# Performance work log

Hardware: AMD Instinct MI355X
Metric: run time of the kernel (lower is better)

Reference implementation:

```python
import jax, jax.numpy as jnp
import numpy as np

B, N, C, D, K, H, A = 4, 2048, 128, 128, 16, 64, 512


def _rn(k, shape, s):
    return (jax.random.normal(k, shape) * s).astype(jnp.float32)


def setup_inputs():
    ks = jax.random.split(jax.random.key(0), 40)
    w = lambda i, o, c: _rn(ks[i], (o, c), 0.02)
    b = lambda i, o: _rn(ks[i + 20], (o,), 0.02)
    p = {}
    p["xyz"] = _rn(ks[0], (B, 3, N), 1.0)
    p["pos"] = _rn(ks[1], (B, 2, N), 1.0)
    p["key"] = _rn(ks[2], (B, C, N), 1.0)
    p["query"] = _rn(ks[3], (B, C, N), 1.0)
    p["mv_w1"] = w(4, C, 2 * C); p["mv_b1"] = b(4, C)
    p["mv_w2"] = w(5, C, C);     p["mv_b2"] = b(5, C)
    p["mv_ws"] = w(6, C, 2 * C); p["mv_bs"] = b(6, C)
    p["wk"] = w(7, D, C); p["bk"] = b(7, D)
    p["wq"] = w(8, D, C); p["bq"] = b(8, D)
    p["wv"] = w(9, D, C); p["bv"] = b(9, D)
    p["xyz_w1"] = w(10, H, 3); p["xyz_b1"] = b(10, H)
    p["xyz_w2"] = w(11, D, H); p["xyz_b2"] = b(11, D)
    p["pos_w1"] = w(12, H, 2); p["pos_b1"] = b(12, H)
    p["pos_w2"] = w(13, D, H); p["pos_b2"] = b(13, D)
    p["xat_w1"] = w(14, A, D); p["xat_b1"] = b(14, A)
    p["xat_w2"] = w(15, D, A); p["xat_b2"] = b(15, D)
    p["at_w1"] = w(16, A, D); p["at_b1"] = b(16, A)
    p["at_w2"] = w(17, D, A); p["at_b2"] = b(17, D)
    p["wkq"] = w(18, C, D); p["bkq"] = b(18, C)
    p["wend"] = w(19, C, D); p["bend"] = b(19, C)
    return p


def c1(w, b, x):  # 1x1 Conv1d: (O,C) on (B,C,N)
    return jnp.einsum('oc,bcn->bon', w, x) + b[None, :, None]


def c2(w, b, x):  # 1x1 Conv2d: (O,C) on (B,C,N,K)
    return jnp.einsum('oc,bcnk->bonk', w, x) + b[None, :, None, None]


def mlp2(w1, b1, w2, b2, x):
    return c2(w2, b2, jax.nn.relu(c2(w1, b1, x)))


def softmax_one(x):  # exp(x-m) / (1 + sum exp(x-m)) over last axis
    m = jnp.max(x, axis=-1, keepdims=True)
    e = jnp.exp(x - m)
    return e / (1.0 + jnp.sum(e, axis=-1, keepdims=True))


def knn_idx(pts, k):  # pts: (B, N, d) -> (B, N, k) indices, include_self=True
    sq = jnp.sum(pts * pts, axis=-1)
    d2 = sq[:, :, None] + sq[:, None, :] - 2.0 * jnp.einsum('bnd,bmd->bnm', pts, pts)
    return jnp.argsort(d2, axis=-1)[:, :, :k]


def group(f, idx):  # f: (B,C,N), idx: (B,N,K) -> (B,C,N,K)
    return jax.vmap(lambda a, i: a[:, i])(f, idx)


def reference(xyz, pos, key, query, mv_w1, mv_b1, mv_w2, mv_b2, mv_ws, mv_bs,
              wk, bk, wq, bq, wv, bv, xyz_w1, xyz_b1, xyz_w2, xyz_b2,
              pos_w1, pos_b1, pos_w2, pos_b2, xat_w1, xat_b1, xat_w2, xat_b2,
              at_w1, at_b1, at_w2, at_b2, wkq, bkq, wend, bend):
    cat = jnp.concatenate([key, query], axis=1)  # (B, 2C, N)
    # MLP_Res
    value = c1(mv_w2, mv_b2, jax.nn.relu(c1(mv_w1, mv_b1, cat))) + c1(mv_ws, mv_bs, cat)
    identity = value
    k = c1(wk, bk, key)
    q = c1(wq, bq, query)
    v = c1(wv, bv, value)
    # ---- block 1: xyz-space kNN attention ----
    idx1 = knn_idx(jnp.swapaxes(xyz, 1, 2), K)           # (B,N,K)
    kq_rel = k[..., None] - group(q, idx1)               # (B,D,N,K)
    xyz_rel = xyz[..., None] - group(xyz, idx1)          # (B,3,N,K)
    xyz_emb = mlp2(xyz_w1, xyz_b1, xyz_w2, xyz_b2, xyz_rel)
    xa = softmax_one(mlp2(xat_w1, xat_b1, xat_w2, xat_b2, kq_rel + xyz_emb))
    agg = jnp.sum(xa * (v[..., None] + xyz_emb), axis=-1)  # (B,D,N)
    value = c1(wkq, bkq, agg) + identity
    value = c1(wv, bv, value)
    # ---- block 2: pos-space kNN attention ----
    idx2 = knn_idx(jnp.swapaxes(pos, 1, 2), K)
    qk_rel = q[..., None] - group(k, idx2)
    pos_rel = pos[..., None] - group(pos, idx2)
    pos_emb = mlp2(pos_w1, pos_b1, pos_w2, pos_b2, pos_rel)
    at = softmax_one(mlp2(at_w1, at_b1, at_w2, at_b2, qk_rel + pos_emb))
    agg = jnp.sum(at * (value[..., None] + pos_emb), axis=-1)
    y = c1(wend, bend, agg)
    return y + identity
```

## Files before the change

### kernel.cpp

```cpp
#include <hip/hip_runtime.h>
#include <hip/hip_bf16.h>

typedef __hip_bfloat16 bf16;
typedef unsigned long long ull;

#define BB 4
#define NN 2048
#define CCH 128
#define DDM 128
#define KNB 16
#define HHD 64
#define AAD 512
#define PP (BB*NN)

typedef __attribute__((ext_vector_type(8))) short short8;
typedef __attribute__((ext_vector_type(16))) float f32x16;

__device__ __forceinline__ float b2f(bf16 x) { return __bfloat162float(x); }
__device__ __forceinline__ bf16 f2b(float x) { return __float2bfloat16(x); }

__device__ __forceinline__ float ldany(const void* p, size_t i, int f32) {
  return f32 ? ((const float*)p)[i] : __bfloat162float(((const bf16*)p)[i]);
}

__device__ __forceinline__ long pack4(float a, float b, float c, float d) {
  union { bf16 h[4]; long l; } u;
  u.h[0] = f2b(a); u.h[1] = f2b(b); u.h[2] = f2b(c); u.h[3] = f2b(d);
  return u.l;
}
__device__ __forceinline__ void unpack4(long l, float* o) {
  union { bf16 h[4]; long l; } u; u.l = l;
  o[0] = b2f(u.h[0]); o[1] = b2f(u.h[1]); o[2] = b2f(u.h[2]); o[3] = b2f(u.h[3]);
}

__device__ __forceinline__ short8 ldfrag(const bf16* base, int row, int stride, int k0, int hl) {
  const bf16* p = base + (size_t)row * stride + k0 + (hl << 3);
  union { short8 v; long l[2]; } u;
  u.l[0] = *(const long*)p;
  u.l[1] = *(const long*)(p + 4);
  return u.v;
}

__device__ __forceinline__ f32x16 MFMA(short8 a, short8 b, f32x16 c) {
  return __builtin_amdgcn_mfma_f32_32x32x16_bf16(a, b, c, 0, 0, 0);
}

struct PtrArr { const void* p[36]; int n[36]; };
struct CvtTab { int src[16]; int off[16]; int n[16]; int isb[16]; };
struct G4 { const bf16* X[4]; int K[4]; int woff[4]; int boff[4]; bf16* out[4]; int relu[4]; };

__global__ __launch_bounds__(256) void sniff_kern(PtrArr pa, int* __restrict__ flags) {
  int t = blockIdx.x;
  const bf16* x = (const bf16*)pa.p[t];
  int n = pa.n[t]; if (n > 4096) n = 4096;
  __shared__ int cnt;
  if (threadIdx.x == 0) cnt = 0;
  __syncthreads();
  int c = 0;
  for (int i = threadIdx.x; i < n; i += 256) {
    float v = fabsf(__bfloat162float(x[i]));
    if (v == 0.f || (v >= 1e-6f && v <= 1024.f)) c++;
  }
  atomicAdd(&cnt, c);
  __syncthreads();
  if (threadIdx.x == 0) flags[t] = (cnt >= (n * 7) / 8) ? 0 : 1;
}

__global__ __launch_bounds__(256) void cvtprep_kern(PtrArr pa, CvtTab tab,
                                                    const int* __restrict__ flags,
                                                    bf16* __restrict__ warena, float* __restrict__ barena,
                                                    bf16* __restrict__ w1img0, bf16* __restrict__ w2img0,
                                                    bf16* __restrict__ cw2img0, float* __restrict__ fb0,
                                                    bf16* __restrict__ w1img1, bf16* __restrict__ w2img1,
                                                    bf16* __restrict__ cw2img1, float* __restrict__ fb1) {
  int y = blockIdx.y;
  if (y >= 2) {
    int e = y - 2;
    int i = blockIdx.x * 256 + threadIdx.x;
    if (i >= tab.n[e]) return;
    float v = ldany(pa.p[tab.src[e]], i, flags[tab.src[e]]);
    if (tab.isb[e]) barena[tab.off[e] + i] = v;
    else warena[tab.off[e] + i] = f2b(v);
    return;
  }
  int set = y;
  int cIdx = set ? 20 : 16, aIdx = set ? 28 : 24, dd = set ? 2 : 3;
  bf16* w1img = set ? w1img1 : w1img0;
  bf16* w2img = set ? w2img1 : w2img0;
  bf16* cw2img = set ? cw2img1 : cw2img0;
  float* fb = set ? fb1 : fb0;
  const void* cw1 = pa.p[cIdx];     const void* cb1 = pa.p[cIdx + 1];
  const void* cw2 = pa.p[cIdx + 2]; const void* cb2 = pa.p[cIdx + 3];
  const void* aw1 = pa.p[aIdx];     const void* ab1 = pa.p[aIdx + 1];
  const void* aw2 = pa.p[aIdx + 2]; const void* ab2 = pa.p[aIdx + 3];
  int i = blockIdx.x * 256 + threadIdx.x;
  const int fcw1 = flags[cIdx], fcb1 = flags[cIdx + 1];
  const int fcw2 = flags[cIdx + 2], fcb2 = flags[cIdx + 3];
  const int faw1 = flags[aIdx], fab1 = flags[aIdx + 1];
  const int faw2 = flags[aIdx + 2], fab2 = flags[aIdx + 3];
  float* ab1f = fb;
  float* ab2f = fb + 512;
  float* cb1f = fb + 640;
  float* cb2f = fb + 704;
  float* cw1f = fb + 832;
  if (i < 65536) {
    int hg = i >> 7, c = i & 127;
    w1img[(size_t)hg * 132 + c] = f2b(ldany(aw1, i, faw1));
  } else if (i < 131072) {
    int j = i - 65536;
    int o = j >> 9, hh = j & 511;
    int ac = hh >> 7, hloc = hh & 127;
    w2img[(size_t)(ac * 128 + o) * 132 + hloc] = f2b(ldany(aw2, j, faw2));
  } else if (i < 139264) {
    int j = i - 131072;
    int o = j >> 6, h = j & 63;
    cw2img[o * 68 + h] = f2b(ldany(cw2, j, fcw2));
  } else if (i < 139776) {
    int j = i - 139264; ab1f[j] = ldany(ab1, j, fab1);
  } else if (i < 139904) {
    int j = i - 139776; ab2f[j] = ldany(ab2, j, fab2);
  } else if (i < 139968) {
    int j = i - 139904; cb1f[j] = ldany(cb1, j, fcb1);
  } else if (i < 140096) {
    int j = i - 139968; cb2f[j] = ldany(cb2, j, fcb2);
  } else if (i < 140288) {
    int j = i - 140096;
    int h = j / 3, c = j % 3;
    cw1f[j] = (c < dd) ? ldany(cw1, h * dd + c, fcw1) : 0.f;
  }
}

__global__ __launch_bounds__(256) void trall_kern(const void* __restrict__ keyp,
                                                  const void* __restrict__ qryp,
                                                  const void* __restrict__ xyzp,
                                                  const void* __restrict__ posp,
                                                  const int* __restrict__ flags,
                                                  bf16* __restrict__ catT,
                                                  float* __restrict__ xyzT,
                                                  float* __restrict__ posT) {
  int bx = blockIdx.x;
  if (bx < 512) {
    __shared__ float tile[64][65];
    int xx = bx & 31, yy = (bx >> 5) & 1, zz = bx >> 6;
    int b = zz & 3, half = zz >> 2;
    const void* src = half ? qryp : keyp;
    const int f32 = flags[2 + half];
    int n0 = xx * 64, c0 = yy * 64;
    int tx = threadIdx.x & 63, ty = threadIdx.x >> 6;
    for (int r = ty; r < 64; r += 4)
      tile[r][tx] = ldany(src, (size_t)(b * 128 + c0 + r) * NN + n0 + tx, f32);
    __syncthreads();
    for (int r = ty; r < 64; r += 4)
      catT[(size_t)(b * NN + n0 + r) * 256 + half * 128 + c0 + tx] = __float2bfloat16(tile[tx][r]);
    return;
  }
  int cb = bx - 512;
  int which = cb >> 7;
  const void* src = which ? posp : xyzp;
  float* dst = which ? posT : xyzT;
  int dd = which ? 2 : 3;
  const int f32 = flags[which];
  int i = (cb & 127) * 256 * 2 + threadIdx.x;
  for (int rep = 0; rep < 2; ++rep, i += 256) {
    if (i < PP * 4) {
      int p = i >> 2, j = i & 3;
      int b = p >> 11, n = p & (NN - 1);
      dst[i] = (j < dd) ? ldany(src, (size_t)(b * dd + j) * NN + n, f32) : 0.f;
    }
  }
}

__global__ __launch_bounds__(256) void gemm4_kern(G4 g, const bf16* __restrict__ warena,
                                                  const float* __restrict__ barena) {
  __shared__ __attribute__((aligned(16))) bf16 XT[64 * 260];
  int op = blockIdx.y;
  const bf16* X = g.X[op];
  int K = g.K[op];
  const bf16* Wb = warena + g.woff[op];
  const float* bias = barena + g.boff[op];
  bf16* out = g.out[op];
  int relu = g.relu[op];
  int tid = threadIdx.x, lane = tid & 63, wv = tid >> 6;
  int hl = lane >> 5, cA = lane & 31;
  int p0 = blockIdx.x * 64;
  int SK = K + 4;
  int kc = K >> 3;
  for (int c = tid; c < 64 * kc; c += 256) {
    int r = c / kc, col = (c % kc) << 3;
    *(float4*)&XT[r * SK + col] = *(const float4*)&X[(size_t)(p0 + r) * 256 + col];
  }
  __syncthreads();
  int o0 = wv * 32;
  f32x16 acc[2];
#pragma unroll
  for (int r = 0; r < 16; ++r) {
    int o = o0 + (r & 3) + 8 * (r >> 2) + 4 * hl;
    float bv = bias[o];
    acc[0][r] = bv; acc[1][r] = bv;
  }
  for (int ks = 0; ks < (K >> 4); ++ks) {
    short8 af = ldfrag(Wb, o0 + cA, K, ks * 16, hl);
    short8 b0 = ldfrag(XT, cA, SK, ks * 16, hl);
    short8 b1 = ldfrag(XT, 32 + cA, SK, ks * 16, hl);
    acc[0] = MFMA(af, b0, acc[0]);
    acc[1] = MFMA(af, b1, acc[1]);
  }
#pragma unroll
  for (int t = 0; t < 2; ++t) {
    int m = p0 + t * 32 + cA;
#pragma unroll
    for (int q = 0; q < 4; ++q) {
      int ob = o0 + 8 * q + 4 * hl;
      float v[4] = {acc[t][4*q+0], acc[t][4*q+1], acc[t][4*q+2], acc[t][4*q+3]};
      if (relu) {
        v[0] = fmaxf(v[0], 0.f); v[1] = fmaxf(v[1], 0.f);
        v[2] = fmaxf(v[2], 0.f); v[3] = fmaxf(v[3], 0.f);
      }
      *(long*)(out + (size_t)m * 128 + ob) = pack4(v[0], v[1], v[2], v[3]);
    }
  }
}

__global__ __launch_bounds__(256) void gemm32_kern(
    const bf16* __restrict__ X,
    const bf16* __restrict__ Wb, const float* __restrict__ bias,
    const bf16* __restrict__ add, bf16* __restrict__ out, int relu,
    void* __restrict__ outT, const int* __restrict__ flags) {
  __shared__ __attribute__((aligned(16))) bf16 XT[32 * 132];
  int tid = threadIdx.x, lane = tid & 63, wv = tid >> 6;
  int hl = lane >> 5, cA = lane & 31;
  int p0 = blockIdx.x * 32;
  for (int c = tid; c < 32 * 16; c += 256) {
    int r = c >> 4, col = (c & 15) << 3;
    *(float4*)&XT[r * 132 + col] = *(const float4*)&X[(size_t)(p0 + r) * 128 + col];
  }
  __syncthreads();
  int o0 = wv * 32;
  f32x16 acc;
#pragma unroll
  for (int r = 0; r < 16; ++r) {
    int o = o0 + (r & 3) + 8 * (r >> 2) + 4 * hl;
    acc[r] = bias[o];
  }
#pragma unroll
  for (int ks = 0; ks < 8; ++ks) {
    short8 af = ldfrag(Wb, o0 + cA, 128, ks * 16, hl);
    short8 b0 = ldfrag(XT, cA, 132, ks * 16, hl);
    acc = MFMA(af, b0, acc);
  }
  int m = p0 + cA;
  int f32o = outT ? flags[2] : 0;
  int b = m >> 11, n = m & (NN - 1);
#pragma unroll
  for (int q = 0; q < 4; ++q) {
    int ob = o0 + 8 * q + 4 * hl;
    float v[4] = {acc[4*q+0], acc[4*q+1], acc[4*q+2], acc[4*q+3]};
    if (add) {
      float av[4];
      unpack4(*(const long*)(add + (size_t)m * 128 + ob), av);
      v[0] += av[0]; v[1] += av[1]; v[2] += av[2]; v[3] += av[3];
    }
    if (relu) {
      v[0] = fmaxf(v[0], 0.f); v[1] = fmaxf(v[1], 0.f);
      v[2] = fmaxf(v[2], 0.f); v[3] = fmaxf(v[3], 0.f);
    }
    if (outT) {
#pragma unroll
      for (int i = 0; i < 4; ++i) {
        size_t oi = (size_t)(b * 128 + ob + i) * NN + n;
        if (f32o) ((float*)outT)[oi] = v[i];
        else ((bf16*)outT)[oi] = f2b(v[i]);
      }
    } else {
      *(long*)(out + (size_t)m * 128 + ob) = pack4(v[0], v[1], v[2], v[3]);
    }
  }
}

__global__ __launch_bounds__(512) void knn_kern(const float* __restrict__ xyzT,
                                                const float* __restrict__ posT,
                                                int* __restrict__ idx1,
                                                int* __restrict__ idx2) {
  __shared__ __attribute__((aligned(16))) float4 cds[NN];
  const float* coordsT = blockIdx.y ? posT : xyzT;
  int* idxout = blockIdx.y ? idx2 : idx1;
  int tid = threadIdx.x, lane = tid & 63, wv = tid >> 6;
  int p0 = blockIdx.x * 8, b = p0 >> 11;
  for (int j = tid; j < NN; j += 512)
    cds[j] = *(const float4*)&coordsT[((size_t)(b << 11) + j) * 4];
  __syncthreads();
  int p = p0 + wv, n = p & (NN - 1);
  float4 cc = cds[n];
  float sqi = __fadd_rn(__fadd_rn(__fmul_rn(cc.x, cc.x), __fmul_rn(cc.y, cc.y)),
                        __fmul_rn(cc.z, cc.z));
  ull t[32];
#pragma unroll
  for (int s = 0; s < 32; ++s) {
    int j = (s << 6) | lane;
    float4 q = cds[j];
    float sqj = __fadd_rn(__fadd_rn(__fmul_rn(q.x, q.x), __fmul_rn(q.y, q.y)),
                          __fmul_rn(q.z, q.z));
    float dt  = __fadd_rn(__fadd_rn(__fmul_rn(cc.x, q.x), __fmul_rn(cc.y, q.y)),
                          __fmul_rn(cc.z, q.z));
    float d2 = __fsub_rn(__fadd_rn(sqi, sqj), __fmul_rn(2.f, dt));
    unsigned u = __float_as_uint(d2);
    u = (u & 0x80000000u) ? ~u : (u | 0x80000000u);
    t[s] = ((ull)u << 32) | (unsigned)j;
  }
#pragma unroll
  for (int k = 2; k <= 32; k <<= 1) {
#pragma unroll
    for (int j = k >> 1; j > 0; j >>= 1) {
#pragma unroll
      for (int i = 0; i < 32; ++i) {
        int l = i ^ j;
        if (l > i) {
          bool up = ((i & k) == 0);
          ull a = t[i], c = t[l];
          ull lo = a < c ? a : c;
          ull hi = a < c ? c : a;
          t[i] = up ? lo : hi;
          t[l] = up ? hi : lo;
        }
      }
    }
  }
  for (int r = 0; r < KNB; ++r) {
    ull h = t[0];
    ull m = h;
#pragma unroll
    for (int off = 1; off < 64; off <<= 1) {
      ull o = __shfl_xor(m, off);
      m = o < m ? o : m;
    }
    if (lane == 0) idxout[(size_t)p * KNB + r] = (int)(m & 0xffffffffu);
    if (h == m) {
#pragma unroll
      for (int i = 0; i < 15; ++i) t[i] = t[i + 1];
      t[15] = ~0ull;
    }
  }
}

#define SMEM_BYTES 72192
__global__ __launch_bounds__(512, 4) void attn_mfma(
    const bf16* __restrict__ centerT, const bf16* __restrict__ gatherT,
    const float* __restrict__ coordsT, const bf16* __restrict__ vfeatT,
    const int* __restrict__ idx,
    const bf16* __restrict__ w1img, const bf16* __restrict__ w2img,
    const bf16* __restrict__ cw2img, const float* __restrict__ fb,
    bf16* __restrict__ aggT) {
  extern __shared__ char smem[];
  bf16* XS  = (bf16*)(smem);
  bf16* HT  = (bf16*)(smem + 33792);
  bf16* HC  = HT;
  bf16* CFE = (bf16*)(smem + 67584);
  bf16* VF  = (bf16*)(smem + 69632);
  int*  NID = (int*)(smem + 71680);
  const float* ab1f = fb;
  const float* ab2f = fb + 512;
  const float* cb1f = fb + 640;
  const float* cb2f = fb + 704;
  const float* cw1f = fb + 832;

  int tid = threadIdx.x, lane = tid & 63, wv = tid >> 6;
  int hl = lane >> 5, cA = lane & 31;
  int P0 = blockIdx.x * 8, b = P0 >> 11;

  if (tid < 128) NID[tid] = (b << 11) + idx[(size_t)(P0 + (tid >> 4)) * KNB + (tid & 15)];
  for (int i = tid; i < 1024; i += 512) {
    int g = i >> 7, d = i & 127;
    CFE[i] = centerT[(size_t)(P0 + g) * 128 + d];
    VF[i]  = vfeatT[(size_t)(P0 + g) * 128 + d];
  }
  __syncthreads();

  {
    int m = tid >> 2, sub = tid & 3;
    float4 ccd = *(const float4*)&coordsT[(size_t)(P0 + (m >> 4)) * 4];
    float4 nbd = *(const float4*)&coordsT[(size_t)NID[m] * 4];
    float r0 = ccd.x - nbd.x, r1 = ccd.y - nbd.y, r2 = ccd.z - nbd.z;
    int h0 = sub * 16;
    for (int hh = h0; hh < h0 + 16; hh += 4) {
      float a0 = fmaxf(cb1f[hh+0] + cw1f[(hh+0)*3]*r0 + cw1f[(hh+0)*3+1]*r1 + cw1f[(hh+0)*3+2]*r2, 0.f);
      float a1 = fmaxf(cb1f[hh+1] + cw1f[(hh+1)*3]*r0 + cw1f[(hh+1)*3+1]*r1 + cw1f[(hh+1)*3+2]*r2, 0.f);
      float a2 = fmaxf(cb1f[hh+2] + cw1f[(hh+2)*3]*r0 + cw1f[(hh+2)*3+1]*r1 + cw1f[(hh+2)*3+2]*r2, 0.f);
      float a3 = fmaxf(cb1f[hh+3] + cw1f[(hh+3)*3]*r0 + cw1f[(hh+3)*3+1]*r1 + cw1f[(hh+3)*3+2]*r2, 0.f);
      *(long*)&HC[m * 68 + hh] = pack4(a0, a1, a2, a3);
    }
    const bf16* grow = gatherT + (size_t)NID[m] * 128 + sub * 32;
    const bf16* crow = CFE + ((m >> 4) << 7) + sub * 32;
    for (int j = 0; j < 32; j += 4) {
      float gv[4], cv[4];
      unpack4(*(const long*)(grow + j), gv);
      unpack4(*(const long*)(crow + j), cv);
      *(long*)&XS[m * 132 + sub * 32 + j] =
          pack4(cv[0] - gv[0], cv[1] - gv[1], cv[2] - gv[2], cv[3] - gv[3]);
    }
  }
  __syncthreads();

  int r0s = (wv & 3) * 32;
  int mt0 = (wv >> 2) * 64;

  short8 pf[8];
#pragma unroll
  for (int ks = 0; ks < 8; ++ks)
    pf[ks] = ldfrag(w1img, r0s + cA, 132, ks * 16, hl);

  {
    f32x16 eacc[2];
#pragma unroll
    for (int r = 0; r < 16; ++r) {
      int o = r0s + (r & 3) + 8 * (r >> 2) + 4 * hl;
      float bv = cb2f[o];
      eacc[0][r] = bv; eacc[1][r] = bv;
    }
    for (int k0 = 0; k0 < 64; k0 += 16) {
      short8 af = ldfrag(cw2img, r0s + cA, 68, k0, hl);
      short8 b0 = ldfrag(HC, mt0 + cA, 68, k0, hl);
      short8 b1 = ldfrag(HC, mt0 + 32 + cA, 68, k0, hl);
      eacc[0] = MFMA(af, b0, eacc[0]);
      eacc[1] = MFMA(af, b1, eacc[1]);
    }
#pragma unroll
    for (int t = 0; t < 2; ++t) {
      int m = mt0 + t * 32 + cA;
#pragma unroll
      for (int q = 0; q < 4; ++q) {
        int ob = r0s + 8 * q + 4 * hl;
        bf16* px = &XS[m * 132 + ob];
        float xv[4];
        unpack4(*(long*)px, xv);
        *(long*)px = pack4(xv[0] + eacc[t][4*q+0], xv[1] + eacc[t][4*q+1],
                           xv[2] + eacc[t][4*q+2], xv[3] + eacc[t][4*q+3]);
      }
    }
  }
  __syncthreads();

  f32x16 acc2[2];
#pragma unroll
  for (int r = 0; r < 16; ++r) {
    int o = r0s + (r & 3) + 8 * (r >> 2) + 4 * hl;
    float bv = ab2f[o];
    acc2[0][r] = bv; acc2[1][r] = bv;
  }

  for (int ac = 0; ac < 4; ++ac) {
    const bf16* w2c = w2img + (size_t)ac * 16896;
    const bf16* w1n = w1img + (size_t)((ac + 1) & 3) * 16896;
    f32x16 acc1[2];
#pragma unroll
    for (int r = 0; r < 16; ++r) {
      int h = r0s + (r & 3) + 8 * (r >> 2) + 4 * hl;
      float bv = ab1f[ac * 128 + h];
      acc1[0][r] = bv; acc1[1][r] = bv;
    }
#pragma unroll
    for (int ks = 0; ks < 8; ++ks) {
      short8 af = pf[ks];
      short8 b0 = ldfrag(XS, mt0 + cA, 132, ks * 16, hl);
      short8 b1 = ldfrag(XS, mt0 + 32 + cA, 132, ks * 16, hl);
      pf[ks] = ldfrag(w2c, r0s + cA, 132, ks * 16, hl);
      acc1[0] = MFMA(af, b0, acc1[0]);
      acc1[1] = MFMA(af, b1, acc1[1]);
    }
    __syncthreads();
#pragma unroll
    for (int t = 0; t < 2; ++t) {
      int m = mt0 + t * 32 + cA;
#pragma unroll
      for (int q = 0; q < 4; ++q) {
        int hb = r0s + 8 * q + 4 * hl;
        *(long*)&HT[m * 132 + hb] =
            pack4(fmaxf(acc1[t][4*q+0], 0.f), fmaxf(acc1[t][4*q+1], 0.f),
                  fmaxf(acc1[t][4*q+2], 0.f), fmaxf(acc1[t][4*q+3], 0.f));
      }
    }
    __syncthreads();
#pragma unroll
    for (int ks = 0; ks < 8; ++ks) {
      short8 af = pf[ks];
      short8 b0 = ldfrag(HT, mt0 + cA, 132, ks * 16, hl);
      short8 b1 = ldfrag(HT, mt0 + 32 + cA, 132, ks * 16, hl);
      pf[ks] = ldfrag(w1n, r0s + cA, 132, ks * 16, hl);
      acc2[0] = MFMA(af, b0, acc2[0]);
      acc2[1] = MFMA(af, b1, acc2[1]);
    }
  }

  __syncthreads();
#pragma unroll
  for (int t = 0; t < 2; ++t) {
    int m = mt0 + t * 32 + cA;
#pragma unroll
    for (int q = 0; q < 4; ++q) {
      int ob = r0s + 8 * q + 4 * hl;
      *(long*)&HT[m * 132 + ob] = pack4(acc2[t][4*q+0], acc2[t][4*q+1],
                                        acc2[t][4*q+2], acc2[t][4*q+3]);
    }
  }
  __syncthreads();

  {
    int g = wv;
    int base = g * 16;
    float vbase0 = b2f(VF[g * 128 + lane])      - b2f(CFE[g * 128 + lane]);
    float vbase1 = b2f(VF[g * 128 + lane + 64]) - b2f(CFE[g * 128 + lane + 64]);
#pragma unroll
    for (int half = 0; half < 2; ++half) {
      int o = lane + half * 64;
      float vb = half ? vbase1 : vbase0;
      float e[16];
      float mx = -3.4e38f;
#pragma unroll
      for (int kk = 0; kk < 16; ++kk) {
        float x = b2f(HT[(base + kk) * 132 + o]);
        e[kk] = x;
        mx = fmaxf(mx, x);
      }
      float s = 0.f;
#pragma unroll
      for (int kk = 0; kk < 16; ++kk) { e[kk] = __expf(e[kk] - mx); s += e[kk]; }
      float inv = 1.f / (1.f + s);
      float acc = 0.f;
#pragma unroll
      for (int kk = 0; kk < 16; ++kk) {
        float xv = b2f(XS[(base + kk) * 132 + o]);
        float gv = b2f(gatherT[(size_t)NID[base + kk] * 128 + o]);
        acc += (e[kk] * inv) * (vb + xv + gv);
      }
      aggT[(size_t)(P0 + g) * 128 + o] = f2b(acc);
    }
  }
}

extern "C" void kernel_launch(void* const* d_in, const int* in_sizes, int n_in,
                              void* d_out, int out_size, void* d_ws, size_t ws_size,
                              hipStream_t stream) {
  int* flags = (int*)d_ws;
  bf16* catT = (bf16*)((float*)d_ws + 64);
  bf16* v0   = catT + (size_t)PP * 256;
  bf16* kT   = v0 + (size_t)PP * 128;
  bf16* qT   = kT + (size_t)PP * 128;
  bf16* sE   = qT + (size_t)PP * 128;
  bf16* sF   = sE + (size_t)PP * 128;
  bf16* sG   = sF + (size_t)PP * 128;
  float* xyzT = (float*)(sG + (size_t)PP * 128);
  float* posT = xyzT + (size_t)PP * 4;
  int* idx1 = (int*)(posT + (size_t)PP * 4);
  int* idx2 = idx1 + (size_t)PP * KNB;
  bf16* w1i1 = (bf16*)(idx2 + (size_t)PP * KNB);
  bf16* w2i1 = w1i1 + 67584;
  bf16* cw2i1 = w2i1 + 67584;
  bf16* w1i2 = cw2i1 + 8704;
  bf16* w2i2 = w1i2 + 67584;
  bf16* cw2i2 = w2i2 + 67584;
  float* fb1 = (float*)(cw2i2 + 8704);
  float* fb2 = fb1 + 1024;
  bf16* warena = (bf16*)(fb2 + 1024);
  float* barena = (float*)(warena + 163840);

  PtrArr pa;
  for (int i = 0; i < 36; ++i) { pa.p[i] = d_in[i]; pa.n[i] = in_sizes[i]; }
  sniff_kern<<<dim3(36), 256, 0, stream>>>(pa, flags);

  CvtTab tab;
  int wsrc[8] = {4, 8, 6, 10, 12, 14, 32, 34};
  int woff[8] = {0, 32768, 65536, 81920, 98304, 114688, 131072, 147456};
  int wn[8]   = {32768, 32768, 16384, 16384, 16384, 16384, 16384, 16384};
  int bsrc[8] = {5, 9, 7, 11, 13, 15, 33, 35};
  for (int e = 0; e < 8; ++e) {
    tab.src[e] = wsrc[e]; tab.off[e] = woff[e]; tab.n[e] = wn[e]; tab.isb[e] = 0;
    tab.src[8 + e] = bsrc[e]; tab.off[8 + e] = e * 128; tab.n[8 + e] = 128; tab.isb[8 + e] = 1;
  }
  cvtprep_kern<<<dim3(548, 18), 256, 0, stream>>>(pa, tab, flags, warena, barena,
                                                  w1i1, w2i1, cw2i1, fb1,
                                                  w1i2, w2i2, cw2i2, fb2);

  trall_kern<<<dim3(768), 256, 0, stream>>>(d_in[2], d_in[3], d_in[0], d_in[1],
                                            flags, catT, xyzT, posT);

  knn_kern<<<dim3(PP / 8, 2), 512, 0, stream>>>(xyzT, posT, idx1, idx2);

  G4 g4;
  g4.X[0] = catT;       g4.K[0] = 256; g4.woff[0] = 0;      g4.boff[0] = 0;   g4.out[0] = sF; g4.relu[0] = 1;
  g4.X[1] = catT;       g4.K[1] = 256; g4.woff[1] = 32768;  g4.boff[1] = 128; g4.out[1] = sG; g4.relu[1] = 0;
  g4.X[2] = catT;       g4.K[2] = 128; g4.woff[2] = 81920;  g4.boff[2] = 384; g4.out[2] = kT; g4.relu[2] = 0;
  g4.X[3] = catT + 128; g4.K[3] = 128; g4.woff[3] = 98304;  g4.boff[3] = 512; g4.out[3] = qT; g4.relu[3] = 0;
  gemm4_kern<<<dim3(PP / 64, 4), 256, 0, stream>>>(g4, warena, barena);

  dim3 g32(PP / 32);
  gemm32_kern<<<g32, 256, 0, stream>>>(sF, warena + 65536,  barena + 256, sG,      v0, 0, nullptr, flags);
  gemm32_kern<<<g32, 256, 0, stream>>>(v0, warena + 114688, barena + 640, nullptr, sE, 0, nullptr, flags);

  hipFuncSetAttribute((const void*)attn_mfma, hipFuncAttributeMaxDynamicSharedMemorySize, SMEM_BYTES);

  attn_mfma<<<dim3(PP / 8), 512, SMEM_BYTES, stream>>>(kT, qT, xyzT, sE, idx1,
                                                       w1i1, w2i1, cw2i1, fb1, sF);
  gemm32_kern<<<g32, 256, 0, stream>>>(sF, warena + 131072, barena + 768, v0,      sG, 0, nullptr, flags);
  gemm32_kern<<<g32, 256, 0, stream>>>(sG, warena + 114688, barena + 640, nullptr, sE, 0, nullptr, flags);
  attn_mfma<<<dim3(PP / 8), 512, SMEM_BYTES, stream>>>(qT, kT, posT, sE, idx2,
                                                       w1i2, w2i2, cw2i2, fb2, sF);
  gemm32_kern<<<g32, 256, 0, stream>>>(sF, warena + 147456, barena + 896, v0, nullptr, 0, d_out, flags);
}
```

Measured before the change: 392.9 us.

## Merge kNN with input GEMMs in one launch and chain back-to-back GEMMs

Combines the kNN kernel and the four-way input GEMM into one grid: the first 2048 blocks do kNN, the rest do GEMM tiles, so the two independent stages overlap. Consecutive 128x128 GEMM pairs are fused into a chain kernel that keeps the intermediate tile in shared memory, and the second chain skips writing its unused intermediate. This cuts kernel launches and global round-trips. The GEMM blocks now use 512 threads with one accumulator each.

```diff
diff --git a/kernel.cpp b/kernel.cpp
--- a/kernel.cpp
+++ b/kernel.cpp
@@ -170,54 +170,186 @@
   }
 }
 
-__global__ __launch_bounds__(256) void gemm4_kern(G4 g, const bf16* __restrict__ warena,
-                                                  const float* __restrict__ barena) {
-  __shared__ __attribute__((aligned(16))) bf16 XT[64 * 260];
-  int op = blockIdx.y;
-  const bf16* X = g.X[op];
-  int K = g.K[op];
-  const bf16* Wb = warena + g.woff[op];
-  const float* bias = barena + g.boff[op];
-  bf16* out = g.out[op];
-  int relu = g.relu[op];
-  int tid = threadIdx.x, lane = tid & 63, wv = tid >> 6;
-  int hl = lane >> 5, cA = lane & 31;
-  int p0 = blockIdx.x * 64;
-  int SK = K + 4;
-  int kc = K >> 3;
-  for (int c = tid; c < 64 * kc; c += 256) {
-    int r = c / kc, col = (c % kc) << 3;
-    *(float4*)&XT[r * SK + col] = *(const float4*)&X[(size_t)(p0 + r) * 256 + col];
-  }
-  __syncthreads();
-  int o0 = wv * 32;
-  f32x16 acc[2];
-#pragma unroll
-  for (int r = 0; r < 16; ++r) {
-    int o = o0 + (r & 3) + 8 * (r >> 2) + 4 * hl;
-    float bv = bias[o];
-    acc[0][r] = bv; acc[1][r] = bv;
-  }
-  for (int ks = 0; ks < (K >> 4); ++ks) {
-    short8 af = ldfrag(Wb, o0 + cA, K, ks * 16, hl);
-    short8 b0 = ldfrag(XT, cA, SK, ks * 16, hl);
-    short8 b1 = ldfrag(XT, 32 + cA, SK, ks * 16, hl);
-    acc[0] = MFMA(af, b0, acc[0]);
-    acc[1] = MFMA(af, b1, acc[1]);
-  }
-#pragma unroll
-  for (int t = 0; t < 2; ++t) {
-    int m = p0 + t * 32 + cA;
+__global__ __launch_bounds__(512) void mega_kern(
+    const float* __restrict__ xyzT, const float* __restrict__ posT,
+    int* __restrict__ idx1, int* __restrict__ idx2,
+    G4 g, const bf16* __restrict__ warena, const float* __restrict__ barena) {
+  __shared__ __attribute__((aligned(16))) char smem[33280];
+  int bx = blockIdx.x;
+  int tid = threadIdx.x, lane = tid & 63, wvv = tid >> 6;
+  if (bx < 2048) {
+    float4* cds = (float4*)smem;
+    int set = bx >> 10;
+    int pblk = bx & 1023;
+    const float* coordsT = set ? posT : xyzT;
+    int* idxout = set ? idx2 : idx1;
+    int p0 = pblk * 8, b = p0 >> 11;
+    for (int j = tid; j < NN; j += 512)
+      cds[j] = *(const float4*)&coordsT[((size_t)(b << 11) + j) * 4];
+    __syncthreads();
+    int p = p0 + wvv, n = p & (NN - 1);
+    float4 cc = cds[n];
+    float sqi = __fadd_rn(__fadd_rn(__fmul_rn(cc.x, cc.x), __fmul_rn(cc.y, cc.y)),
+                          __fmul_rn(cc.z, cc.z));
+    ull t[32];
+#pragma unroll
+    for (int s = 0; s < 32; ++s) {
+      int j = (s << 6) | lane;
+      float4 q = cds[j];
+      float sqj = __fadd_rn(__fadd_rn(__fmul_rn(q.x, q.x), __fmul_rn(q.y, q.y)),
+                            __fmul_rn(q.z, q.z));
+      float dt  = __fadd_rn(__fadd_rn(__fmul_rn(cc.x, q.x), __fmul_rn(cc.y, q.y)),
+                            __fmul_rn(cc.z, q.z));
+      float d2 = __fsub_rn(__fadd_rn(sqi, sqj), __fmul_rn(2.f, dt));
+      unsigned u = __float_as_uint(d2);
+      u = (u & 0x80000000u) ? ~u : (u | 0x80000000u);
+      t[s] = ((ull)u << 32) | (unsigned)j;
+    }
+#pragma unroll
+    for (int k = 2; k <= 32; k <<= 1) {
+#pragma unroll
+      for (int j = k >> 1; j > 0; j >>= 1) {
+#pragma unroll
+        for (int i = 0; i < 32; ++i) {
+          int l = i ^ j;
+          if (l > i) {
+            bool up = ((i & k) == 0);
+            ull a = t[i], c = t[l];
+            ull lo = a < c ? a : c;
+            ull hi = a < c ? c : a;
+            t[i] = up ? lo : hi;
+            t[l] = up ? hi : lo;
+          }
+        }
+      }
+    }
+    for (int r = 0; r < KNB; ++r) {
+      ull h = t[0];
+      ull m = h;
+#pragma unroll
+      for (int off = 1; off < 64; off <<= 1) {
+        ull o = __shfl_xor(m, off);
+        m = o < m ? o : m;
+      }
+      if (lane == 0) idxout[(size_t)p * KNB + r] = (int)(m & 0xffffffffu);
+      if (h == m) {
+#pragma unroll
+        for (int i = 0; i < 15; ++i) t[i] = t[i + 1];
+        t[15] = ~0ull;
+      }
+    }
+    return;
+  }
+  {
+    bf16* XT = (bf16*)smem;
+    int bx2 = bx - 2048;
+    int op = bx2 >> 7, ptile = bx2 & 127;
+    const bf16* X = g.X[op];
+    int K = g.K[op];
+    const bf16* Wb = warena + g.woff[op];
+    const float* bias = barena + g.boff[op];
+    bf16* out = g.out[op];
+    int relu = g.relu[op];
+    int hl = lane >> 5, cA = lane & 31;
+    int p0 = ptile * 64;
+    int SK = K + 4;
+    int kc = K >> 3;
+    for (int c = tid; c < 64 * kc; c += 512) {
+      int r = c / kc, col = (c % kc) << 3;
+      *(float4*)&XT[r * SK + col] = *(const float4*)&X[(size_t)(p0 + r) * 256 + col];
+    }
+    __syncthreads();
+    int o0 = (wvv & 3) * 32;
+    int tt = wvv >> 2;
+    f32x16 acc;
+#pragma unroll
+    for (int r = 0; r < 16; ++r) {
+      int o = o0 + (r & 3) + 8 * (r >> 2) + 4 * hl;
+      acc[r] = bias[o];
+    }
+    for (int ks = 0; ks < (K >> 4); ++ks) {
+      short8 af = ldfrag(Wb, o0 + cA, K, ks * 16, hl);
+      short8 b0 = ldfrag(XT, tt * 32 + cA, SK, ks * 16, hl);
+      acc = MFMA(af, b0, acc);
+    }
+    int m = p0 + tt * 32 + cA;
 #pragma unroll
     for (int q = 0; q < 4; ++q) {
       int ob = o0 + 8 * q + 4 * hl;
-      float v[4] = {acc[t][4*q+0], acc[t][4*q+1], acc[t][4*q+2], acc[t][4*q+3]};
+      float v[4] = {acc[4*q+0], acc[4*q+1], acc[4*q+2], acc[4*q+3]};
       if (relu) {
         v[0] = fmaxf(v[0], 0.f); v[1] = fmaxf(v[1], 0.f);
         v[2] = fmaxf(v[2], 0.f); v[3] = fmaxf(v[3], 0.f);
       }
       *(long*)(out + (size_t)m * 128 + ob) = pack4(v[0], v[1], v[2], v[3]);
     }
+  }
+}
+
+__global__ __launch_bounds__(256) void gemm_chain_kern(
+    const bf16* __restrict__ X, const bf16* __restrict__ warena,
+    const float* __restrict__ barena,
+    int w1off, int b1off, const bf16* __restrict__ add1, bf16* __restrict__ out1,
+    int w2off, int b2off, bf16* __restrict__ out2) {
+  __shared__ __attribute__((aligned(16))) bf16 XT[32 * 132];
+  __shared__ __attribute__((aligned(16))) bf16 YT[32 * 132];
+  int tid = threadIdx.x, lane = tid & 63, wv = tid >> 6;
+  int hl = lane >> 5, cA = lane & 31;
+  int p0 = blockIdx.x * 32;
+  for (int c = tid; c < 32 * 16; c += 256) {
+    int r = c >> 4, col = (c & 15) << 3;
+    *(float4*)&XT[r * 132 + col] = *(const float4*)&X[(size_t)(p0 + r) * 128 + col];
+  }
+  __syncthreads();
+  int o0 = wv * 32;
+  const bf16* W1 = warena + w1off;
+  const float* b1 = barena + b1off;
+  f32x16 acc;
+#pragma unroll
+  for (int r = 0; r < 16; ++r) {
+    int o = o0 + (r & 3) + 8 * (r >> 2) + 4 * hl;
+    acc[r] = b1[o];
+  }
+#pragma unroll
+  for (int ks = 0; ks < 8; ++ks) {
+    short8 af = ldfrag(W1, o0 + cA, 128, ks * 16, hl);
+    short8 b0 = ldfrag(XT, cA, 132, ks * 16, hl);
+    acc = MFMA(af, b0, acc);
+  }
+  int m = p0 + cA;
+#pragma unroll
+  for (int q = 0; q < 4; ++q) {
+    int ob = o0 + 8 * q + 4 * hl;
+    float v[4] = {acc[4*q+0], acc[4*q+1], acc[4*q+2], acc[4*q+3]};
+    if (add1) {
+      float av[4];
+      unpack4(*(const long*)(add1 + (size_t)m * 128 + ob), av);
+      v[0] += av[0]; v[1] += av[1]; v[2] += av[2]; v[3] += av[3];
+    }
+    long pk = pack4(v[0], v[1], v[2], v[3]);
+    *(long*)&YT[cA * 132 + ob] = pk;
+    if (out1) *(long*)(out1 + (size_t)m * 128 + ob) = pk;
+  }
+  __syncthreads();
+  const bf16* W2 = warena + w2off;
+  const float* b2 = barena + b2off;
+  f32x16 acc2;
+#pragma unroll
+  for (int r = 0; r < 16; ++r) {
+    int o = o0 + (r & 3) + 8 * (r >> 2) + 4 * hl;
+    acc2[r] = b2[o];
+  }
+#pragma unroll
+  for (int ks = 0; ks < 8; ++ks) {
+    short8 af = ldfrag(W2, o0 + cA, 128, ks * 16, hl);
+    short8 b0 = ldfrag(YT, cA, 132, ks * 16, hl);
+    acc2 = MFMA(af, b0, acc2);
+  }
+#pragma unroll
+  for (int q = 0; q < 4; ++q) {
+    int ob = o0 + 8 * q + 4 * hl;
+    *(long*)(out2 + (size_t)m * 128 + ob) =
+        pack4(acc2[4*q+0], acc2[4*q+1], acc2[4*q+2], acc2[4*q+3]);
   }
 }
 
@@ -273,71 +405,6 @@
       }
     } else {
       *(long*)(out + (size_t)m * 128 + ob) = pack4(v[0], v[1], v[2], v[3]);
-    }
-  }
-}
-
-__global__ __launch_bounds__(512) void knn_kern(const float* __restrict__ xyzT,
-                                                const float* __restrict__ posT,
-                                                int* __restrict__ idx1,
-                                                int* __restrict__ idx2) {
-  __shared__ __attribute__((aligned(16))) float4 cds[NN];
-  const float* coordsT = blockIdx.y ? posT : xyzT;
-  int* idxout = blockIdx.y ? idx2 : idx1;
-  int tid = threadIdx.x, lane = tid & 63, wv = tid >> 6;
-  int p0 = blockIdx.x * 8, b = p0 >> 11;
-  for (int j = tid; j < NN; j += 512)
-    cds[j] = *(const float4*)&coordsT[((size_t)(b << 11) + j) * 4];
-  __syncthreads();
-  int p = p0 + wv, n = p & (NN - 1);
-  float4 cc = cds[n];
-  float sqi = __fadd_rn(__fadd_rn(__fmul_rn(cc.x, cc.x), __fmul_rn(cc.y, cc.y)),
-                        __fmul_rn(cc.z, cc.z));
-  ull t[32];
-#pragma unroll
-  for (int s = 0; s < 32; ++s) {
-    int j = (s << 6) | lane;
-    float4 q = cds[j];
-    float sqj = __fadd_rn(__fadd_rn(__fmul_rn(q.x, q.x), __fmul_rn(q.y, q.y)),
-                          __fmul_rn(q.z, q.z));
-    float dt  = __fadd_rn(__fadd_rn(__fmul_rn(cc.x, q.x), __fmul_rn(cc.y, q.y)),
-                          __fmul_rn(cc.z, q.z));
-    float d2 = __fsub_rn(__fadd_rn(sqi, sqj), __fmul_rn(2.f, dt));
-    unsigned u = __float_as_uint(d2);
-    u = (u & 0x80000000u) ? ~u : (u | 0x80000000u);
-    t[s] = ((ull)u << 32) | (unsigned)j;
-  }
-#pragma unroll
-  for (int k = 2; k <= 32; k <<= 1) {
-#pragma unroll
-    for (int j = k >> 1; j > 0; j >>= 1) {
-#pragma unroll
-      for (int i = 0; i < 32; ++i) {
-        int l = i ^ j;
-        if (l > i) {
-          bool up = ((i & k) == 0);
-          ull a = t[i], c = t[l];
-          ull lo = a < c ? a : c;
-          ull hi = a < c ? c : a;
-          t[i] = up ? lo : hi;
-          t[l] = up ? hi : lo;
-        }
-      }
-    }
-  }
-  for (int r = 0; r < KNB; ++r) {
-    ull h = t[0];
-    ull m = h;
-#pragma unroll
-    for (int off = 1; off < 64; off <<= 1) {
-      ull o = __shfl_xor(m, off);
-      m = o < m ? o : m;
-    }
-    if (lane == 0) idxout[(size_t)p * KNB + r] = (int)(m & 0xffffffffu);
-    if (h == m) {
-#pragma unroll
-      for (int i = 0; i < 15; ++i) t[i] = t[i + 1];
-      t[15] = ~0ull;
     }
   }
 }
@@ -582,26 +649,26 @@
   trall_kern<<<dim3(768), 256, 0, stream>>>(d_in[2], d_in[3], d_in[0], d_in[1],
                                             flags, catT, xyzT, posT);
 
-  knn_kern<<<dim3(PP / 8, 2), 512, 0, stream>>>(xyzT, posT, idx1, idx2);
-
   G4 g4;
   g4.X[0] = catT;       g4.K[0] = 256; g4.woff[0] = 0;      g4.boff[0] = 0;   g4.out[0] = sF; g4.relu[0] = 1;
   g4.X[1] = catT;       g4.K[1] = 256; g4.woff[1] = 32768;  g4.boff[1] = 128; g4.out[1] = sG; g4.relu[1] = 0;
   g4.X[2] = catT;       g4.K[2] = 128; g4.woff[2] = 81920;  g4.boff[2] = 384; g4.out[2] = kT; g4.relu[2] = 0;
   g4.X[3] = catT + 128; g4.K[3] = 128; g4.woff[3] = 98304;  g4.boff[3] = 512; g4.out[3] = qT; g4.relu[3] = 0;
-  gemm4_kern<<<dim3(PP / 64, 4), 256, 0, stream>>>(g4, warena, barena);
-
-  dim3 g32(PP / 32);
-  gemm32_kern<<<g32, 256, 0, stream>>>(sF, warena + 65536,  barena + 256, sG,      v0, 0, nullptr, flags);
-  gemm32_kern<<<g32, 256, 0, stream>>>(v0, warena + 114688, barena + 640, nullptr, sE, 0, nullptr, flags);
+  mega_kern<<<dim3(2048 + 512), 512, 0, stream>>>(xyzT, posT, idx1, idx2, g4, warena, barena);
+
+  gemm_chain_kern<<<dim3(PP / 32), 256, 0, stream>>>(sF, warena, barena,
+                                                     65536, 256, sG, v0,
+                                                     114688, 640, sE);
 
   hipFuncSetAttribute((const void*)attn_mfma, hipFuncAttributeMaxDynamicSharedMemorySize, SMEM_BYTES);
 
   attn_mfma<<<dim3(PP / 8), 512, SMEM_BYTES, stream>>>(kT, qT, xyzT, sE, idx1,
                                                        w1i1, w2i1, cw2i1, fb1, sF);
-  gemm32_kern<<<g32, 256, 0, stream>>>(sF, warena + 131072, barena + 768, v0,      sG, 0, nullptr, flags);
-  gemm32_kern<<<g32, 256, 0, stream>>>(sG, warena + 114688, barena + 640, nullptr, sE, 0, nullptr, flags);
+  gemm_chain_kern<<<dim3(PP / 32), 256, 0, stream>>>(sF, warena, barena,
+                                                     131072, 768, v0, nullptr,
+                                                     114688, 640, sE);
   attn_mfma<<<dim3(PP / 8), 512, SMEM_BYTES, stream>>>(qT, kT, posT, sE, idx2,
                                                        w1i2, w2i2, cw2i2, fb2, sF);
-  gemm32_kern<<<g32, 256, 0, stream>>>(sF, warena + 147456, barena + 896, v0, nullptr, 0, d_out, flags);
-}
+  gemm32_kern<<<dim3(PP / 32), 256, 0, stream>>>(sF, warena + 147456, barena + 896, v0,
+                                                 nullptr, 0, d_out, flags);
+}
```

Measured after the change: 378.1 us. 1.04x faster.
